# Kernel tuning notes

Hardware: AMD Instinct MI355X
Metric: run time of the kernel (lower is better)

Reference implementation:

```python
import jax, jax.numpy as jnp
import numpy as np

NUM_SLOTS = 16
CORE_INPUT_SIZE = 256


def _perm_matrix(key):
    p = jax.random.permutation(key, NUM_SLOTS)
    return jnp.eye(NUM_SLOTS, dtype=jnp.float32)[p]


def setup_inputs() -> dict:
    key = jax.random.key(0)
    kx, k1, k2 = jax.random.split(key, 3)
    x = jax.random.normal(kx, (512, 16, 16, CORE_INPUT_SIZE), dtype=jnp.float32)
    Ppos = _perm_matrix(k1)
    Pneg = _perm_matrix(k2)
    return {"x": x, "Ppos": Ppos, "Pneg": Pneg}


def reference(x, Ppos, Pneg):
    B, O, I, C = x.shape
    # split last dim into (num_slots rows, cols)
    xr = x.reshape(B, O, I, NUM_SLOTS, C // NUM_SLOTS)
    # permutation-matrix einsum on the slots axis (a one-hot gather)
    xpos = jnp.einsum('ij,boijk->boiik'.replace('boij', 'bOIj').replace('boii', 'bOIi'), Ppos, xr) if False else jnp.einsum('ij,...jk->...ik', Ppos, xr)
    xneg = jnp.einsum('ij,...jk->...ik', Pneg, xr)
    return (xpos - xneg).reshape(B, O, I, C)
```

## Files before the change

kernel.cpp:

```cpp
#include <hip/hip_runtime.h>


#define NSLOTS 16

__global__ __launch_bounds__(256) void permute_ws_kernel(
    const float4* __restrict__ x,
    const float* __restrict__ Ppos,
    const float* __restrict__ Pneg,
    float4* __restrict__ out,
    long total_v4)
{
    __shared__ int spos[NSLOTS];
    __shared__ int sneg[NSLOTS];

    const int t = threadIdx.x;
    if (t < NSLOTS) {
        int ip = 0, in_ = 0;
        #pragma unroll
        for (int j = 0; j < NSLOTS; ++j) {
            if (Ppos[t * NSLOTS + j] > 0.5f) ip = j;
            if (Pneg[t * NSLOTS + j] > 0.5f) in_ = j;
        }
        spos[t] = ip;
        sneg[t] = in_;
    }
    __syncthreads();

    long idx = (long)blockIdx.x * blockDim.x + threadIdx.x;
    const long stride = (long)gridDim.x * blockDim.x;

    for (; idx < total_v4; idx += stride) {
        const long row_base = idx & ~63L;
        const int  v        = (int)(idx & 63);
        const int  slot     = v >> 2;
        const int  k4       = v & 3;

        const float4 a = x[row_base + ((long)spos[slot] << 2) + k4];
        const float4 b = x[row_base + ((long)sneg[slot] << 2) + k4];

        float4 r;
        r.x = a.x - b.x;
        r.y = a.y - b.y;
        r.z = a.z - b.z;
        r.w = a.w - b.w;
        out[idx] = r;
    }
}

extern "C" void kernel_launch(void* const* d_in, const int* in_sizes, int n_in,
                              void* d_out, int out_size, void* d_ws, size_t ws_size,
                              hipStream_t stream)
{
    const float4* x    = (const float4*)d_in[0];
    const float*  Ppos = (const float*)d_in[1];
    const float*  Pneg = (const float*)d_in[2];
    float4*       out  = (float4*)d_out;

    const long total_v4 = (long)out_size / 4;

    const int block = 256;
    long blocks_needed = (total_v4 + block - 1) / block;
    int grid = (int)(blocks_needed > 32768 ? 32768 : blocks_needed);

    permute_ws_kernel<<<grid, block, 0, stream>>>(x, Ppos, Pneg, out, total_v4);
}
```

Baseline: 223.6 us.

## Unroll grid-stride loop 4x with hoisted offsets and nontemporal stores

```diff
diff --git a/kernel.cpp b/kernel.cpp
--- a/kernel.cpp
+++ b/kernel.cpp
@@ -3,15 +3,17 @@
 
 #define NSLOTS 16
 
-__global__ __launch_bounds__(256) void permute_ws_kernel(
-    const float4* __restrict__ x,
+typedef float fvec4 __attribute__((ext_vector_type(4)));
+
+__global__ __launch_bounds__(256, 8) void permute_ws_kernel(
+    const fvec4* __restrict__ x,
     const float* __restrict__ Ppos,
     const float* __restrict__ Pneg,
-    float4* __restrict__ out,
+    fvec4* __restrict__ out,
     long total_v4)
 {
-    __shared__ int spos[NSLOTS];
-    __shared__ int sneg[NSLOTS];
+    __shared__ int soff_p[NSLOTS];
+    __shared__ int soff_n[NSLOTS];
 
     const int t = threadIdx.x;
     if (t < NSLOTS) {
@@ -21,29 +23,44 @@
             if (Ppos[t * NSLOTS + j] > 0.5f) ip = j;
             if (Pneg[t * NSLOTS + j] > 0.5f) in_ = j;
         }
-        spos[t] = ip;
-        sneg[t] = in_;
+        soff_p[t] = ip << 2;
+        soff_n[t] = in_ << 2;
     }
     __syncthreads();
 
     long idx = (long)blockIdx.x * blockDim.x + threadIdx.x;
-    const long stride = (long)gridDim.x * blockDim.x;
+    const long stride = (long)gridDim.x * (long)blockDim.x;
 
-    for (; idx < total_v4; idx += stride) {
-        const long row_base = idx & ~63L;
-        const int  v        = (int)(idx & 63);
-        const int  slot     = v >> 2;
-        const int  k4       = v & 3;
+    const int v    = (int)(idx & 63);
+    const int slot = v >> 2;
+    const int k4   = v & 3;
+    const long dp = (long)(soff_p[slot] + k4 - v);
+    const long dn = (long)(soff_n[slot] + k4 - v);
 
-        const float4 a = x[row_base + ((long)spos[slot] << 2) + k4];
-        const float4 b = x[row_base + ((long)sneg[slot] << 2) + k4];
-
-        float4 r;
-        r.x = a.x - b.x;
-        r.y = a.y - b.y;
-        r.z = a.z - b.z;
-        r.w = a.w - b.w;
-        out[idx] = r;
+    long i = idx;
+    for (; i + 3 * stride < total_v4; i += 4 * stride) {
+        const fvec4 a0 = x[i              + dp];
+        const fvec4 b0 = x[i              + dn];
+        const fvec4 a1 = x[i +     stride + dp];
+        const fvec4 b1 = x[i +     stride + dn];
+        const fvec4 a2 = x[i + 2 * stride + dp];
+        const fvec4 b2 = x[i + 2 * stride + dn];
+        const fvec4 a3 = x[i + 3 * stride + dp];
+        const fvec4 b3 = x[i + 3 * stride + dn];
+        const fvec4 r0 = a0 - b0;
+        const fvec4 r1 = a1 - b1;
+        const fvec4 r2 = a2 - b2;
+        const fvec4 r3 = a3 - b3;
+        __builtin_nontemporal_store(r0, &out[i]);
+        __builtin_nontemporal_store(r1, &out[i +     stride]);
+        __builtin_nontemporal_store(r2, &out[i + 2 * stride]);
+        __builtin_nontemporal_store(r3, &out[i + 3 * stride]);
+    }
+    for (; i < total_v4; i += stride) {
+        const fvec4 a = x[i + dp];
+        const fvec4 b = x[i + dn];
+        const fvec4 r = a - b;
+        __builtin_nontemporal_store(r, &out[i]);
     }
 }
 
@@ -51,16 +68,16 @@
                               void* d_out, int out_size, void* d_ws, size_t ws_size,
                               hipStream_t stream)
 {
-    const float4* x    = (const float4*)d_in[0];
-    const float*  Ppos = (const float*)d_in[1];
-    const float*  Pneg = (const float*)d_in[2];
-    float4*       out  = (float4*)d_out;
+    const fvec4* x    = (const fvec4*)d_in[0];
+    const float* Ppos = (const float*)d_in[1];
+    const float* Pneg = (const float*)d_in[2];
+    fvec4*       out  = (fvec4*)d_out;
 
     const long total_v4 = (long)out_size / 4;
 
     const int block = 256;
     long blocks_needed = (total_v4 + block - 1) / block;
-    int grid = (int)(blocks_needed > 32768 ? 32768 : blocks_needed);
+    int grid = (int)(blocks_needed > 2048 ? 2048 : blocks_needed);
 
     permute_ws_kernel<<<grid, block, 0, stream>>>(x, Ppos, Pneg, out, total_v4);
 }
```

New measurement: 239.1 us. +6.9%, slower.
